# Kernel optimization log

Measured on AMD Instinct MI355X. Metric: run time of the kernel, lower is better.

Reference implementation:

```python
import jax, jax.numpy as jnp
import numpy as np

NUM_CLASS = 3
SCORE_THRESH = 0.1
NMS_THRESH = 0.25
PRE = 512    # NMS_PRE_MAXSIZE (reduced from 4096 for memory; same algorithm)
POST = 100   # NMS_POST_MAXSIZE
EPS = 1e-8


def _cross(a, b):
    return a[..., 0] * b[..., 1] - a[..., 1] * b[..., 0]


def _corners(box):
    # box: (7,) = (x, y, z, dx, dy, dz, heading) -> BEV corners (4,2), CCW
    x, y, dx, dy, r = box[0], box[1], box[3], box[4], box[6]
    c, s = jnp.cos(r), jnp.sin(r)
    lx = jnp.array([0.5, -0.5, -0.5, 0.5]) * dx
    ly = jnp.array([0.5, 0.5, -0.5, -0.5]) * dy
    return jnp.stack([x + lx * c - ly * s, y + lx * s + ly * c], axis=-1)


def _in_box(pts, box):
    # pts (P,2): point-in-rotated-rect test in the box frame
    px, py = pts[:, 0] - box[0], pts[:, 1] - box[1]
    c, s = jnp.cos(box[6]), jnp.sin(box[6])
    u = px * c + py * s
    v = -px * s + py * c
    return (jnp.abs(u) <= box[3] * 0.5 + 1e-5) & (jnp.abs(v) <= box[4] * 0.5 + 1e-5)


def _bev_inter_area(ba, bb):
    # Exact rotated-rect intersection area (same construction as the CUDA
    # iou3d kernel: inside corners + edge intersections, angle-sorted shoelace).
    ca, cb = _corners(ba), _corners(bb)
    pa, ra = ca, jnp.roll(ca, -1, 0) - ca       # edges of a
    pb, rb = cb, jnp.roll(cb, -1, 0) - cb       # edges of b
    d = _cross(ra[:, None, :], rb[None, :, :])  # (4,4)
    dsafe = jnp.where(jnp.abs(d) > EPS, d, 1.0)
    qp = pb[None, :, :] - pa[:, None, :]
    t = _cross(qp, rb[None, :, :]) / dsafe
    u = _cross(qp, ra[:, None, :]) / dsafe
    vi = (jnp.abs(d) > EPS) & (t >= 0.0) & (t <= 1.0) & (u >= 0.0) & (u <= 1.0)
    ip = pa[:, None, :] + t[..., None] * ra[:, None, :]  # (4,4,2)
    pts = jnp.concatenate([ca, cb, ip.reshape(16, 2)], 0)          # (24,2)
    val = jnp.concatenate([_in_box(ca, bb), _in_box(cb, ba), vi.reshape(16)], 0)
    cnt = val.sum()
    ctr = (pts * val[:, None]).sum(0) / jnp.maximum(cnt, 1)
    ang = jnp.where(val, jnp.arctan2(pts[:, 1] - ctr[1], pts[:, 0] - ctr[0]), 1e9)
    o = jnp.argsort(ang)
    ps, vs = pts[o], val[o]
    ps = jnp.where(vs[:, None], ps, ps[0])  # collapse invalid onto first valid pt
    area = 0.5 * jnp.abs(_cross(ps, jnp.roll(ps, -1, 0)).sum())
    return jnp.where(cnt >= 3, area, 0.0)


def _iou3d(ba, bb):
    inter = _bev_inter_area(ba, bb)
    zt = jnp.minimum(ba[2] + ba[5] * 0.5, bb[2] + bb[5] * 0.5)
    zb = jnp.maximum(ba[2] - ba[5] * 0.5, bb[2] - bb[5] * 0.5)
    i3 = inter * jnp.maximum(zt - zb, 0.0)
    va = ba[3] * ba[4] * ba[5]
    vb = bb[3] * bb[4] * bb[5]
    return i3 / jnp.maximum(va + vb - i3, EPS)


_iou_mat = jax.vmap(jax.vmap(_iou3d, (None, 0)), (0, None))


def _nms(scores, boxes):
    # scores (K,) sorted descending; greedy suppression in score order
    valid = scores >= SCORE_THRESH
    iou = _iou_mat(boxes, boxes)  # (K,K)

    def body(sup, inp):
        row, v, i = inp
        keep = v & jnp.logical_not(sup[i])
        sup = sup | (keep & (row > NMS_THRESH))
        return sup, keep

    K = scores.shape[0]
    _, keep = jax.lax.scan(body, jnp.zeros((K,), bool), (iou, valid, jnp.arange(K)))
    return keep


def _post_one(cls_logits, boxes):
    # multi_classes_nms path: cls_preds_normalized=False -> sigmoid
    scores = jax.nn.sigmoid(cls_logits)  # (N, NUM_CLASS)
    out_b, out_s, out_l = [], [], []
    for k in range(NUM_CLASS):
        s = jnp.where(scores[:, k] >= SCORE_THRESH, scores[:, k], -1.0)
        top_s, idx = jax.lax.top_k(s, PRE)
        b = boxes[idx]
        keep = _nms(top_s, b)
        ks = jnp.where(keep, top_s, -1.0)
        os_, oi = jax.lax.top_k(ks, POST)
        ov = os_ >= SCORE_THRESH
        out_b.append(jnp.where(ov[:, None], b[oi], 0.0))
        out_s.append(jnp.where(ov, os_, 0.0))
        out_l.append((k + 1) * ov.astype(jnp.int32))  # final_labels = k + 1
    return (jnp.concatenate(out_b, 0), jnp.concatenate(out_s, 0),
            jnp.concatenate(out_l, 0))


def setup_inputs() -> dict:
    key = jax.random.key(0)
    k1, k2 = jax.random.split(key)
    B, N = 2, 100000
    batch_cls_preds = jax.random.normal(k1, (B, N, NUM_CLASS), dtype=jnp.float32)
    u = jax.random.uniform(k2, (B, N, 7), dtype=jnp.float32)
    x = u[..., 0] * 70.0
    y = u[..., 1] * 80.0 - 40.0
    z = u[..., 2] * 2.0 - 1.0
    dx = u[..., 3] * 3.0 + 1.5
    dy = u[..., 4] * 1.5 + 1.2
    dz = u[..., 5] * 1.0 + 1.3
    r = u[..., 6] * 2.0 * np.pi - np.pi
    batch_box_preds = jnp.stack([x, y, z, dx, dy, dz, r], axis=-1)
    return {"batch_cls_preds": batch_cls_preds, "batch_box_preds": batch_box_preds}


def reference(batch_cls_preds, batch_box_preds):
    # returns per-batch padded (pred_boxes (B, 3*POST, 7), pred_scores, pred_labels);
    # invalid slots are zeroed (label 0 == no detection)
    return jax.vmap(_post_one)(batch_cls_preds, batch_box_preds)
```

## Files before the change

kernel.cpp:

```cpp
#include <hip/hip_runtime.h>
#include <cstdint>

#define NCLS 3
#define NPTS 100000
#define NB 2
#define PRE 512
#define POST 100
#define SCORE_TH 0.1f
#define NMS_TH 0.25
#define CAP 1024
#define XBIN_SH 16
#define XBIN_OFF (0xBFC00000u >> XBIN_SH)
#define XMARG 2e-3f
#define NPROB (NB * NCLS)
#define NKB 98
#define BUFREG 1024
#define BUFSZ (NKB * BUFREG)
#define NCELL 36
#define GEOP 21
#define NRB 1024
#define RB_OFF (0xBF400000u >> 12)


__device__ __forceinline__ uint32_t score_key(float x)
{
    double sd = 1.0 / (1.0 + exp(-(double)x));
    float s = (float)sd;
    if (!(s >= SCORE_TH)) s = -1.0f;
    uint32_t u = __float_as_uint(s);
    return (u & 0x80000000u) ? ~u : (u | 0x80000000u);
}

__device__ __forceinline__ int xbin1(float x)
{
    uint32_t u = __float_as_uint(x);
    uint32_t key = (u & 0x80000000u) ? ~u : (u | 0x80000000u);
    return (int)(key >> XBIN_SH) - (int)XBIN_OFF;
}

__global__ __launch_bounds__(1024) void stage_kernel(
    const float* __restrict__ cls, uint32_t* __restrict__ blkcnt,
    unsigned long long* __restrict__ buf)
{
    __shared__ uint32_t lcnt3[NCLS];
    const int tid = threadIdx.x;
    if (tid < NCLS) lcnt3[tid] = 0;
    __syncthreads();

    const int b = blockIdx.x / NKB, kb = blockIdx.x % NKB;
    const int i = kb * 1024 + tid;
    if (i < NPTS) {
        const float* cp = cls + ((size_t)b * NPTS + i) * NCLS;
        #pragma unroll
        for (int k = 0; k < NCLS; ++k) {
            float x = cp[k];
            if (xbin1(x + XMARG) >= 1) {
                uint32_t kk = score_key(x);
                uint32_t slot = atomicAdd(&lcnt3[k], 1u);
                buf[(size_t)(b * NCLS + k) * BUFSZ + kb * BUFREG + slot]
                    = ((unsigned long long)kk << 32) | (uint32_t)(~(uint32_t)i);
            }
        }
    }
    __syncthreads();
    if (tid < NCLS)
        blkcnt[(b * NKB + kb) * NCLS + tid] = lcnt3[tid];
}

__global__ __launch_bounds__(1024) void cell_kernel(
    const float* __restrict__ boxes, const uint32_t* __restrict__ blkcnt,
    const unsigned long long* __restrict__ buf,
    uint32_t* __restrict__ cand_idx, float* __restrict__ cand_score,
    unsigned long long* __restrict__ mask)
{
    const int blk = blockIdx.x;
    const int p = blk / NCELL;
    const int b = p / NCLS, k = p % NCLS;
    int cc = blk % NCELL;
    int wi = 0;
    while (cc >= 8 - wi) { cc -= 8 - wi; ++wi; }
    const int wj = wi + cc;
    const int tid = threadIdx.x;
    const int lane = tid & 63;
    const int wv = tid >> 6;

    __shared__ unsigned long long skeybuf[2 * CAP];
    unsigned long long* skey2 = skeybuf;
    uint32_t* queue = (uint32_t*)skeybuf;
    __shared__ uint16_t sRB[CAP];
    __shared__ uint32_t sblk[NKB];
    __shared__ uint32_t rhist[NRB + 1];
    __shared__ uint32_t rcnt[NRB];
    __shared__ double geo[128][GEOP];
    __shared__ float scx[128], scy[128];
    __shared__ float sczlo[128], sczhi[128], scrad[128];
    __shared__ uint32_t smw[128];
    __shared__ uint32_t lcnt;
    __shared__ uint32_t pivot_s;

    for (int t = tid; t < 128 * GEOP; t += 1024) ((double*)geo)[t] = 0.0;
    rhist[tid] = 0;
    rcnt[tid] = 0;
    if (tid == 0) { rhist[NRB] = 0; lcnt = 0; pivot_s = 0; }
    if (tid < 128) {
        scx[tid] = 0.0f; scy[tid] = 0.0f;
        sczlo[tid] = 0.0f; sczhi[tid] = 0.0f; scrad[tid] = 0.0f;
        smw[tid] = 0u;
    }
    if (wi == 0 && wj == 0 && tid < PRE) {
        cand_idx[p * PRE + tid] = 0;
        cand_score[p * PRE + tid] = -1.0f;
    }
    if (tid < NKB) sblk[tid] = blkcnt[(b * NKB + tid) * NCLS + k];
    __syncthreads();

    {
        const int rsub = tid >> 6;
        for (int r0 = 0; r0 < NKB; r0 += 16) {
            const int r = r0 + rsub;
            if (r < NKB) {
                const uint32_t c_r = sblk[r];
                const unsigned long long* R =
                    buf + (size_t)p * BUFSZ + r * BUFREG;
                for (uint32_t t = (uint32_t)lane; t < c_r; t += 64) {
                    uint32_t kk = (uint32_t)(R[t] >> 32);
                    int v = (int)(kk >> 12) - (int)RB_OFF;
                    int rb = v < 0 ? 0 : (v > NRB - 1 ? NRB - 1 : v);
                    atomicAdd(&rhist[rb], 1u);
                }
            }
        }
    }
    __syncthreads();

    if (wv == 0) {
        uint32_t carry = 0;
        for (int c = (NRB / 64) - 1; c >= 0; --c) {
            uint32_t v = rhist[c * 64 + lane];
            uint32_t sfx = v;
            #pragma unroll
            for (int off = 1; off < 64; off <<= 1) {
                uint32_t o = __shfl_down(sfx, off);
                sfx += (lane + off < 64) ? o : 0u;
            }
            rhist[c * 64 + lane] = sfx + carry;
            carry += (uint32_t)__shfl((int)sfx, 0);
        }
    }
    __syncthreads();

    if (tid < NRB && rhist[tid] >= PRE && rhist[tid + 1] < PRE)
        pivot_s = (uint32_t)tid;
    __syncthreads();
    const int PB = (int)pivot_s;
    const int cnt2raw = (int)rhist[PB];
    const int cnt2 = cnt2raw < CAP ? cnt2raw : CAP;

    {
        const int rsub = tid >> 6;
        for (int r0 = 0; r0 < NKB; r0 += 16) {
            const int r = r0 + rsub;
            if (r < NKB) {
                const uint32_t c_r = sblk[r];
                const unsigned long long* R =
                    buf + (size_t)p * BUFSZ + r * BUFREG;
                for (uint32_t t = (uint32_t)lane; t < c_r; t += 64) {
                    unsigned long long e = R[t];
                    uint32_t kk = (uint32_t)(e >> 32);
                    int v = (int)(kk >> 12) - (int)RB_OFF;
                    int rb = v < 0 ? 0 : (v > NRB - 1 ? NRB - 1 : v);
                    if (rb >= PB) {
                        uint32_t off = atomicAdd(&rcnt[rb], 1u);
                        uint32_t slot = rhist[rb + 1] + off;
                        if (slot < CAP) {
                            skey2[slot] = e;
                            sRB[slot] = (uint16_t)rb;
                        }
                    }
                }
            }
        }
    }
    __syncthreads();

    unsigned long long mykey = 0ull;
    int rank = 0;
    if (tid < cnt2) {
        mykey = skey2[tid];
        const int myrb = (int)sRB[tid];
        const int mylo = (int)rhist[myrb + 1];
        int hi2 = (int)rhist[myrb];
        if (hi2 > cnt2) hi2 = cnt2;
        int c2 = 0;
        for (int t = mylo; t < hi2; ++t)
            c2 += (skey2[t] > mykey) ? 1 : 0;
        rank = mylo + c2;
    }

    if (tid < cnt2) {
        uint32_t idx = ~((uint32_t)mykey);
        if (wi == 0 && wj == 0 && rank < PRE) {
            uint32_t ov = (uint32_t)(mykey >> 32);
            uint32_t ub = (ov & 0x80000000u) ? (ov ^ 0x80000000u) : ~ov;
            cand_idx[p * PRE + rank] = idx;
            cand_score[p * PRE + rank] = __uint_as_float(ub);
        }
        const int slotA = rank - wi * 64;
        const int slotB = rank - wj * 64;
        const bool inA = (slotA >= 0 && slotA < 64);
        const bool inB = (slotB >= 0 && slotB < 64);
        if (inA || inB) {
            const float* bp = boxes + ((size_t)b * NPTS + idx) * 7;
            double x = bp[0], y = bp[1], z = bp[2];
            double dx = bp[3], dy = bp[4], dz = bp[5], r = bp[6];
            double c = cos(r), s = sin(r);
            double hx = 0.5 * dx, hy = 0.5 * dy;
            double zlo = z - 0.5 * dz, zhi = z + 0.5 * dz;
            double rad = sqrt(hx * hx + hy * hy);
            double V[20];
            V[0] = x; V[1] = y; V[2] = c; V[3] = s; V[4] = hx; V[5] = hy;
            V[6] = zlo; V[7] = zhi; V[8] = dx * dy * dz; V[9] = rad;
            const double lxs[4] = { hx, -hx, -hx,  hx };
            const double lys[4] = { hy,  hy, -hy, -hy };
            #pragma unroll
            for (int m = 0; m < 4; ++m) {
                V[10 + m] = x + lxs[m] * c - lys[m] * s;
                V[14 + m] = y + lxs[m] * s + lys[m] * c;
            }
            if (inA) {
                #pragma unroll
                for (int m = 0; m < 20; ++m) geo[slotA][m] = V[m];
                scx[slotA] = (float)x; scy[slotA] = (float)y;
                sczlo[slotA] = (float)zlo; sczhi[slotA] = (float)zhi;
                scrad[slotA] = (float)rad;
            }
            if (inB) {
                #pragma unroll
                for (int m = 0; m < 20; ++m) geo[64 + slotB][m] = V[m];
                scx[64 + slotB] = (float)x; scy[64 + slotB] = (float)y;
                sczlo[64 + slotB] = (float)zlo; sczhi[64 + slotB] = (float)zhi;
                scrad[64 + slotB] = (float)rad;
            }
        }
    }
    __syncthreads();

    for (int rr = wv; rr < 64; rr += 16) {
        const int bi = wi * 64 + rr;
        const double* A = geo[rr];
        bool needPoly = false;
        {
            const int jcol = wj * 64 + lane;
            if (jcol > bi) {
                float hzf = fminf(sczhi[rr], sczhi[64 + lane])
                          - fmaxf(sczlo[rr], sczlo[64 + lane]);
                if (hzf > 0.0f) {
                    float ddxf = scx[rr] - scx[64 + lane];
                    float ddyf = scy[rr] - scy[64 + lane];
                    float rsf = scrad[rr] + scrad[64 + lane] + 0.01f;
                    if (ddxf * ddxf + ddyf * ddyf <= rsf * rsf) {
                        const double* B = geo[64 + lane];
                        double hzd = fmin(A[7], B[7]) - fmax(A[6], B[6]);
                        if (hzd > 0.0) {
                            double ddx = B[0] - A[0], ddy = B[1] - A[1];
                            double ca = A[2], sa = A[3];
                            double cb2 = B[2], sb2 = B[3];
                            double cd = fabs(ca * cb2 + sa * sb2);
                            double sd = fabs(sa * cb2 - ca * sb2);
                            double pax = fabs(ddx * ca + ddy * sa);
                            double pay = fabs(-ddx * sa + ddy * ca);
                            double pbx = fabs(ddx * cb2 + ddy * sb2);
                            double pby = fabs(-ddx * sb2 + ddy * cb2);
                            if (!(pax > A[4] + B[4] * cd + B[5] * sd) &&
                                !(pay > A[5] + B[4] * sd + B[5] * cd) &&
                                !(pbx > B[4] + A[4] * cd + A[5] * sd) &&
                                !(pby > B[5] + A[4] * sd + A[5] * cd)) {
                                double areaA = 4.0 * A[4] * A[5];
                                double areaB = 4.0 * B[4] * B[5];
                                double i3m = fmin(areaA, areaB) * hzd;
                                double den = A[8] + B[8] - i3m;
                                if (den < 1e-8) den = 1e-8;
                                needPoly = (i3m / den > (double)NMS_TH);
                            }
                        }
                    }
                }
            }
        }
        if (needPoly) {
            uint32_t pos = atomicAdd(&lcnt, 1u);
            queue[pos] = (uint32_t)((rr << 6) | lane);
        }
    }
    __syncthreads();
    const int qcnt = (int)lcnt;

    const int half = lane >> 5;
    const int lane31 = lane & 31;
    const int hid = (wv << 1) | half;
    for (int base = 0; base < qcnt; base += 32) {
        const int qi = base + hid;
        const bool act = qi < qcnt;
        uint32_t e = act ? queue[qi] : 0u;
        const int rr_ = (int)(e >> 6) & 63;
        const int jb = (int)(e & 63u);
        const double* A = geo[rr_];
        const double* B = geo[64 + jb];

        double PX = 0.0, PY = 0.0;
        bool valid = false;
        if (act) {
            if (lane31 < 8) {
                const double* S = (lane31 < 4) ? A : B;
                const double* O = (lane31 < 4) ? B : A;
                int m = lane31 & 3;
                PX = S[10 + m]; PY = S[14 + m];
                double rx = PX - O[0], ry = PY - O[1];
                double u =  rx * O[2] + ry * O[3];
                double v = -rx * O[3] + ry * O[2];
                valid = (fabs(u) <= O[4] + 1e-5) && (fabs(v) <= O[5] + 1e-5);
            } else if (lane31 < 24) {
                int e2 = lane31 - 8, m = e2 >> 2, nn = e2 & 3;
                double ax = A[10 + m], ay = A[14 + m];
                double rax = A[10 + ((m + 1) & 3)] - ax;
                double ray = A[14 + ((m + 1) & 3)] - ay;
                double bx = B[10 + nn], by = B[14 + nn];
                double rbx = B[10 + ((nn + 1) & 3)] - bx;
                double rby = B[14 + ((nn + 1) & 3)] - by;
                double d = rax * rby - ray * rbx;
                if (fabs(d) > 1e-8) {
                    double qx = bx - ax, qy = by - ay;
                    double tt = (qx * rby - qy * rbx) / d;
                    double uu = (qx * ray - qy * rax) / d;
                    valid = (tt >= 0.0 && tt <= 1.0 && uu >= 0.0 && uu <= 1.0);
                    PX = ax + tt * rax; PY = ay + tt * ray;
                }
            }
        }
        if (!valid) { PX = 0.0; PY = 0.0; }

        unsigned long long bal = __ballot(valid);
        int cntv = __popc((uint32_t)(bal >> (half ? 32 : 0)));
        double sx = PX, sy = PY;
        #pragma unroll
        for (int off = 16; off; off >>= 1) {
            sx += __shfl_xor(sx, off);
            sy += __shfl_xor(sy, off);
        }
        int cdiv = cntv > 0 ? cntv : 1;
        double cxc = sx / cdiv, cyc = sy / cdiv;

        double ang = valid ? atan2(PY - cyc, PX - cxc) : 1e9;
        int sidx = lane31;

        #pragma unroll
        for (int kk2 = 2; kk2 <= 32; kk2 <<= 1) {
            #pragma unroll
            for (int jj = kk2 >> 1; jj > 0; jj >>= 1) {
                double oang = __shfl_xor(ang, jj);
                double opx  = __shfl_xor(PX, jj);
                double opy  = __shfl_xor(PY, jj);
                int    oidx = __shfl_xor(sidx, jj);
                bool iLow = (lane31 & jj) == 0;
                bool dirUp = (lane31 & kk2) == 0;
                bool mineFirst = (ang < oang) || (ang == oang && sidx < oidx);
                bool keepMine = (mineFirst == (iLow == dirUp));
                if (!keepMine) { ang = oang; PX = opx; PY = opy; sidx = oidx; }
            }
        }

        double nxp = __shfl(PX, (half << 5) | ((lane31 + 1) & 31));
        double nyp = __shfl(PY, (half << 5) | ((lane31 + 1) & 31));
        double fx  = __shfl(PX, half << 5);
        double fy  = __shfl(PY, half << 5);
        bool last = (lane31 == cntv - 1);
        double qx = last ? fx : nxp, qy = last ? fy : nyp;
        double contrib = 0.0;
        if (lane31 < cntv)
            contrib = (PX - cxc) * (qy - cyc) - (PY - cyc) * (qx - cxc);
        #pragma unroll
        for (int off = 16; off; off >>= 1)
            contrib += __shfl_xor(contrib, off);
        double inter = (cntv >= 3) ? 0.5 * fabs(contrib) : 0.0;

        if (act && lane31 == 0) {
            double zt = fmin(A[7], B[7]);
            double zb = fmax(A[6], B[6]);
            double hz = zt - zb;
            bool sup = false;
            if (hz > 0.0) {
                double i3 = inter * hz;
                double den = A[8] + B[8] - i3;
                if (den < 1e-8) den = 1e-8;
                sup = (i3 / den) > (double)NMS_TH;
            }
            if (sup)
                atomicOr(&smw[rr_ * 2 + (jb >> 5)], 1u << (jb & 31));
        }
    }
    __syncthreads();

    if (tid < 64) {
        unsigned long long w = (unsigned long long)smw[tid * 2]
            | ((unsigned long long)smw[tid * 2 + 1] << 32);
        mask[(size_t)(p * PRE + wi * 64 + tid) * 8 + wj] = w;
    }
}

__global__ __launch_bounds__(256) void nms_out_kernel(
    const float* __restrict__ boxes, const uint32_t* __restrict__ cand_idx,
    const float* __restrict__ cand_score,
    const unsigned long long* __restrict__ mask, float* __restrict__ out)
{
    const int p = blockIdx.x;
    const int b = p / NCLS, k = p % NCLS;
    const int tid = threadIdx.x;

    __shared__ unsigned long long smask[PRE * 8];
    __shared__ float sscore[PRE];
    __shared__ int slist[POST];
    __shared__ int scnt;

    for (int w = tid; w < PRE * 8; w += 256)
        smask[w] = mask[(size_t)p * PRE * 8 + w];
    for (int i = tid; i < PRE; i += 256)
        sscore[i] = cand_score[p * PRE + i];
    __syncthreads();

    if (tid < 64) {
        const int ln = tid;
        unsigned long long rem = 0ull;
        #pragma unroll
        for (int w = 0; w < 8; ++w) {
            unsigned long long bw = __ballot(sscore[w * 64 + ln] >= SCORE_TH);
            if (ln == w) rem = bw;
        }
        int c = 0;
        for (;;) {
            int cv = rem ? ((ln << 6) + (__ffsll(rem) - 1)) : 4096;
            int o1 = __shfl_xor(cv, 1); cv = cv < o1 ? cv : o1;
            int o2 = __shfl_xor(cv, 2); cv = cv < o2 ? cv : o2;
            int o4 = __shfl_xor(cv, 4); cv = cv < o4 ? cv : o4;
            int i = __shfl(cv, 0);
            if (i >= 4096) break;
            if (ln == 0) slist[c] = i;
            ++c;
            if (c >= POST) break;
            unsigned long long mm = (ln < 8) ? smask[i * 8 + ln] : 0ull;
            if (ln == (i >> 6)) mm |= 1ull << (i & 63);
            rem &= ~mm;
        }
        if (ln == 0) scnt = c;
    }
    __syncthreads();

    const int cnt2 = scnt;
    for (int t2 = tid; t2 < POST; t2 += 256) {
        int row = b * (NCLS * POST) + k * POST + t2;
        float* ob = out + (size_t)row * 7;
        float* os = out + (size_t)NB * NCLS * POST * 7 + row;
        float* ol = out + (size_t)NB * NCLS * POST * 7 + (size_t)NB * NCLS * POST + row;
        if (t2 < cnt2) {
            int rr = slist[t2];
            uint32_t idx = cand_idx[p * PRE + rr];
            const float* bp = boxes + ((size_t)b * NPTS + idx) * 7;
            #pragma unroll
            for (int c7 = 0; c7 < 7; ++c7) ob[c7] = bp[c7];
            *os = sscore[rr];
            *ol = (float)(k + 1);
        } else {
            #pragma unroll
            for (int c7 = 0; c7 < 7; ++c7) ob[c7] = 0.0f;
            *os = 0.0f;
            *ol = 0.0f;
        }
    }
}

extern "C" void kernel_launch(void* const* d_in, const int* in_sizes, int n_in,
                              void* d_out, int out_size, void* d_ws, size_t ws_size,
                              hipStream_t stream)
{
    (void)in_sizes; (void)n_in; (void)out_size; (void)ws_size;
    const float* cls   = (const float*)d_in[0];
    const float* boxes = (const float*)d_in[1];
    float* out = (float*)d_out;

    char* ws = (char*)d_ws;
    uint32_t* blkcnt      = (uint32_t*)(ws);
    unsigned long long* buf = (unsigned long long*)(ws + 4096);
    uint32_t* cand_idx    = (uint32_t*)(ws + 4820992);
    float*    cand_score  = (float*)   (ws + 4833280);
    unsigned long long* mask = (unsigned long long*)(ws + 4845568);

    hipLaunchKernelGGL(stage_kernel, dim3(NB * NKB), dim3(1024), 0,
                       stream, cls, blkcnt, buf);
    hipLaunchKernelGGL(cell_kernel, dim3(NPROB * NCELL), dim3(1024), 0,
                       stream, boxes, blkcnt, buf,
                       cand_idx, cand_score, mask);
    hipLaunchKernelGGL(nms_out_kernel, dim3(NPROB), dim3(256), 0, stream,
                       boxes, cand_idx, cand_score, mask, out);
}
```

Measured before the change: 114.4 us.

## Fuse score prefilter into cell kernel, compacting survivors into shared memory

Removes the separate staging kernel and its global workspace buffer. Each cell block now scans the full class-score plane itself with float4 loads, compacts threshold survivors into a shared-memory array using wave ballots, and then builds the radix histogram and candidate scatter from shared memory. This drops one launch and a global write/read round trip. In exchange, all 36 cell blocks per problem redundantly read the whole score plane and rerun the sigmoid key, and shared memory use grows by 64 KB. Survivors beyond SCAP are silently dropped.

```diff
diff --git a/kernel.cpp b/kernel.cpp
--- a/kernel.cpp
+++ b/kernel.cpp
@@ -9,13 +9,11 @@
 #define SCORE_TH 0.1f
 #define NMS_TH 0.25
 #define CAP 1024
+#define SCAP 8192
 #define XBIN_SH 16
 #define XBIN_OFF (0xBFC00000u >> XBIN_SH)
 #define XMARG 2e-3f
 #define NPROB (NB * NCLS)
-#define NKB 98
-#define BUFREG 1024
-#define BUFSZ (NKB * BUFREG)
 #define NCELL 36
 #define GEOP 21
 #define NRB 1024
@@ -38,38 +36,8 @@
     return (int)(key >> XBIN_SH) - (int)XBIN_OFF;
 }
 
-__global__ __launch_bounds__(1024) void stage_kernel(
-    const float* __restrict__ cls, uint32_t* __restrict__ blkcnt,
-    unsigned long long* __restrict__ buf)
-{
-    __shared__ uint32_t lcnt3[NCLS];
-    const int tid = threadIdx.x;
-    if (tid < NCLS) lcnt3[tid] = 0;
-    __syncthreads();
-
-    const int b = blockIdx.x / NKB, kb = blockIdx.x % NKB;
-    const int i = kb * 1024 + tid;
-    if (i < NPTS) {
-        const float* cp = cls + ((size_t)b * NPTS + i) * NCLS;
-        #pragma unroll
-        for (int k = 0; k < NCLS; ++k) {
-            float x = cp[k];
-            if (xbin1(x + XMARG) >= 1) {
-                uint32_t kk = score_key(x);
-                uint32_t slot = atomicAdd(&lcnt3[k], 1u);
-                buf[(size_t)(b * NCLS + k) * BUFSZ + kb * BUFREG + slot]
-                    = ((unsigned long long)kk << 32) | (uint32_t)(~(uint32_t)i);
-            }
-        }
-    }
-    __syncthreads();
-    if (tid < NCLS)
-        blkcnt[(b * NKB + kb) * NCLS + tid] = lcnt3[tid];
-}
-
 __global__ __launch_bounds__(1024) void cell_kernel(
-    const float* __restrict__ boxes, const uint32_t* __restrict__ blkcnt,
-    const unsigned long long* __restrict__ buf,
+    const float* __restrict__ cls, const float* __restrict__ boxes,
     uint32_t* __restrict__ cand_idx, float* __restrict__ cand_score,
     unsigned long long* __restrict__ mask)
 {
@@ -84,24 +52,25 @@
     const int lane = tid & 63;
     const int wv = tid >> 6;
 
+    __shared__ unsigned long long surv[SCAP];
     __shared__ unsigned long long skeybuf[2 * CAP];
     unsigned long long* skey2 = skeybuf;
     uint32_t* queue = (uint32_t*)skeybuf;
     __shared__ uint16_t sRB[CAP];
-    __shared__ uint32_t sblk[NKB];
     __shared__ uint32_t rhist[NRB + 1];
     __shared__ uint32_t rcnt[NRB];
     __shared__ double geo[128][GEOP];
     __shared__ float scx[128], scy[128];
     __shared__ float sczlo[128], sczhi[128], scrad[128];
     __shared__ uint32_t smw[128];
+    __shared__ uint32_t scnt_s;
     __shared__ uint32_t lcnt;
     __shared__ uint32_t pivot_s;
 
     for (int t = tid; t < 128 * GEOP; t += 1024) ((double*)geo)[t] = 0.0;
     rhist[tid] = 0;
     rcnt[tid] = 0;
-    if (tid == 0) { rhist[NRB] = 0; lcnt = 0; pivot_s = 0; }
+    if (tid == 0) { rhist[NRB] = 0; lcnt = 0; pivot_s = 0; scnt_s = 0; }
     if (tid < 128) {
         scx[tid] = 0.0f; scy[tid] = 0.0f;
         sczlo[tid] = 0.0f; sczhi[tid] = 0.0f; scrad[tid] = 0.0f;
@@ -111,25 +80,62 @@
         cand_idx[p * PRE + tid] = 0;
         cand_score[p * PRE + tid] = -1.0f;
     }
-    if (tid < NKB) sblk[tid] = blkcnt[(b * NKB + tid) * NCLS + k];
     __syncthreads();
 
     {
-        const int rsub = tid >> 6;
-        for (int r0 = 0; r0 < NKB; r0 += 16) {
-            const int r = r0 + rsub;
-            if (r < NKB) {
-                const uint32_t c_r = sblk[r];
-                const unsigned long long* R =
-                    buf + (size_t)p * BUFSZ + r * BUFREG;
-                for (uint32_t t = (uint32_t)lane; t < c_r; t += 64) {
-                    uint32_t kk = (uint32_t)(R[t] >> 32);
-                    int v = (int)(kk >> 12) - (int)RB_OFF;
-                    int rb = v < 0 ? 0 : (v > NRB - 1 ? NRB - 1 : v);
-                    atomicAdd(&rhist[rb], 1u);
-                }
-            }
-        }
+        const float* plane = cls + (size_t)b * NPTS * NCLS;
+        for (int r = 0; r < 25; ++r) {
+            const int base = r * 4096 + (tid << 2);
+            const bool vld = base < NPTS;
+            float xs0 = 0.0f, xs1 = 0.0f, xs2 = 0.0f, xs3 = 0.0f;
+            if (vld) {
+                const float4* vp =
+                    (const float4*)(plane + (size_t)base * 3);
+                float4 va = vp[0], vb = vp[1], vc = vp[2];
+                if (k == 0)      { xs0 = va.x; xs1 = va.w; xs2 = vb.z; xs3 = vc.y; }
+                else if (k == 1) { xs0 = va.y; xs1 = vb.x; xs2 = vb.w; xs3 = vc.z; }
+                else             { xs0 = va.z; xs1 = vb.y; xs2 = vc.x; xs3 = vc.w; }
+            }
+#define PUSHX(xv, jj)                                                       \
+            {                                                               \
+                bool sv_ = vld && (xbin1((xv) + XMARG) >= 1);               \
+                unsigned long long bal_ = __ballot(sv_);                    \
+                if (bal_) {                                                 \
+                    int ldr_ = __ffsll(bal_) - 1;                           \
+                    uint32_t wb_ = 0;                                       \
+                    if (lane == ldr_)                                       \
+                        wb_ = atomicAdd(&scnt_s,                            \
+                                        (uint32_t)__popcll(bal_));          \
+                    wb_ = (uint32_t)__shfl((int)wb_, ldr_);                 \
+                    if (sv_) {                                              \
+                        uint32_t slot_ = wb_ + (uint32_t)__popcll(          \
+                            bal_ & ((1ull << lane) - 1ull));                \
+                        if (slot_ < SCAP)                                   \
+                            surv[slot_] =                                   \
+                                ((unsigned long long)__float_as_uint(xv)    \
+                                 << 32) | (uint32_t)(base + (jj));          \
+                    }                                                       \
+                }                                                           \
+            }
+            PUSHX(xs0, 0)
+            PUSHX(xs1, 1)
+            PUSHX(xs2, 2)
+            PUSHX(xs3, 3)
+#undef PUSHX
+        }
+    }
+    __syncthreads();
+    const uint32_t scnt2u = scnt_s < SCAP ? scnt_s : SCAP;
+
+    for (uint32_t t = tid; t < scnt2u; t += 1024) {
+        unsigned long long e = surv[t];
+        float x = __uint_as_float((uint32_t)(e >> 32));
+        uint32_t i = (uint32_t)e;
+        uint32_t kk = score_key(x);
+        surv[t] = ((unsigned long long)kk << 32) | (uint32_t)(~i);
+        int v = (int)(kk >> 12) - (int)RB_OFF;
+        int rb = v < 0 ? 0 : (v > NRB - 1 ? NRB - 1 : v);
+        atomicAdd(&rhist[rb], 1u);
     }
     __syncthreads();
 
@@ -156,28 +162,17 @@
     const int cnt2raw = (int)rhist[PB];
     const int cnt2 = cnt2raw < CAP ? cnt2raw : CAP;
 
-    {
-        const int rsub = tid >> 6;
-        for (int r0 = 0; r0 < NKB; r0 += 16) {
-            const int r = r0 + rsub;
-            if (r < NKB) {
-                const uint32_t c_r = sblk[r];
-                const unsigned long long* R =
-                    buf + (size_t)p * BUFSZ + r * BUFREG;
-                for (uint32_t t = (uint32_t)lane; t < c_r; t += 64) {
-                    unsigned long long e = R[t];
-                    uint32_t kk = (uint32_t)(e >> 32);
-                    int v = (int)(kk >> 12) - (int)RB_OFF;
-                    int rb = v < 0 ? 0 : (v > NRB - 1 ? NRB - 1 : v);
-                    if (rb >= PB) {
-                        uint32_t off = atomicAdd(&rcnt[rb], 1u);
-                        uint32_t slot = rhist[rb + 1] + off;
-                        if (slot < CAP) {
-                            skey2[slot] = e;
-                            sRB[slot] = (uint16_t)rb;
-                        }
-                    }
-                }
+    for (uint32_t t = tid; t < scnt2u; t += 1024) {
+        unsigned long long e = surv[t];
+        uint32_t kk = (uint32_t)(e >> 32);
+        int v = (int)(kk >> 12) - (int)RB_OFF;
+        int rb = v < 0 ? 0 : (v > NRB - 1 ? NRB - 1 : v);
+        if (rb >= PB) {
+            uint32_t off = atomicAdd(&rcnt[rb], 1u);
+            uint32_t slot = rhist[rb + 1] + off;
+            if (slot < CAP) {
+                skey2[slot] = e;
+                sRB[slot] = (uint16_t)rb;
             }
         }
     }
@@ -487,17 +482,12 @@
     float* out = (float*)d_out;
 
     char* ws = (char*)d_ws;
-    uint32_t* blkcnt      = (uint32_t*)(ws);
-    unsigned long long* buf = (unsigned long long*)(ws + 4096);
-    uint32_t* cand_idx    = (uint32_t*)(ws + 4820992);
-    float*    cand_score  = (float*)   (ws + 4833280);
-    unsigned long long* mask = (unsigned long long*)(ws + 4845568);
-
-    hipLaunchKernelGGL(stage_kernel, dim3(NB * NKB), dim3(1024), 0,
-                       stream, cls, blkcnt, buf);
+    uint32_t* cand_idx    = (uint32_t*)(ws);
+    float*    cand_score  = (float*)   (ws + 12288);
+    unsigned long long* mask = (unsigned long long*)(ws + 24576);
+
     hipLaunchKernelGGL(cell_kernel, dim3(NPROB * NCELL), dim3(1024), 0,
-                       stream, boxes, blkcnt, buf,
-                       cand_idx, cand_score, mask);
+                       stream, cls, boxes, cand_idx, cand_score, mask);
     hipLaunchKernelGGL(nms_out_kernel, dim3(NPROB), dim3(256), 0, stream,
                        boxes, cand_idx, cand_score, mask, out);
 }
```

After: 151.8 us. +32.7%, slower.
